# Performance work log

Measured on AMD Instinct MI355X. Metric: run time of the kernel, lower is better.

## Reference

```python
import jax, jax.numpy as jnp
from jax import lax
import numpy as np

D_MODEL = 1024
D_STATE = 16
D_CONV = 4
EXPAND = 2
D_INNER = EXPAND * D_MODEL          # 2048
DT_RANK = (D_MODEL + 15) // 16      # 64
B_SZ, SEQ = 2, 2048


def setup_inputs() -> dict:
    key = jax.random.key(0)
    ks = jax.random.split(key, 10)
    s = 0.02
    x = jax.random.normal(ks[0], (B_SZ, SEQ, D_MODEL), jnp.float32)
    ln_w = jnp.ones((D_MODEL,), jnp.float32)
    ln_b = jnp.zeros((D_MODEL,), jnp.float32)
    in_proj_w = jax.random.normal(ks[1], (2 * D_INNER, D_MODEL), jnp.float32) * s
    conv_w = jax.random.normal(ks[2], (D_INNER, 1, D_CONV), jnp.float32) * s
    conv_b = jnp.zeros((D_INNER,), jnp.float32)
    x_proj_w = jax.random.normal(ks[3], (DT_RANK + 2 * D_STATE, D_INNER), jnp.float32) * s
    dt_proj_w = jax.random.normal(ks[4], (D_INNER, DT_RANK), jnp.float32) * s
    dt_proj_b = jax.random.normal(ks[5], (D_INNER,), jnp.float32) * s
    # standard Mamba S4D-real init: A = -[1..d_state] per channel
    A_log = jnp.log(jnp.tile(jnp.arange(1, D_STATE + 1, dtype=jnp.float32), (D_INNER, 1)))
    D_param = jnp.ones((D_INNER,), jnp.float32)
    out_proj_w = jax.random.normal(ks[6], (D_MODEL, D_INNER), jnp.float32) * s
    return dict(x=x, ln_w=ln_w, ln_b=ln_b, in_proj_w=in_proj_w, conv_w=conv_w,
                conv_b=conv_b, x_proj_w=x_proj_w, dt_proj_w=dt_proj_w,
                dt_proj_b=dt_proj_b, A_log=A_log, D_param=D_param,
                out_proj_w=out_proj_w)


def _mamba_layer(x, ln_w, ln_b, in_proj_w, conv_w, conv_b, x_proj_w,
                 dt_proj_w, dt_proj_b, A_log, D_param, out_proj_w):
    # LayerNorm (eps=1e-5)
    mu = x.mean(-1, keepdims=True)
    var = ((x - mu) ** 2).mean(-1, keepdims=True)
    xn = (x - mu) * lax.rsqrt(var + 1e-5) * ln_w + ln_b

    # input projection -> gate + conv branch
    xz = jnp.einsum('bld,ed->ble', xn, in_proj_w)  # [B,L,2*D_INNER]
    x_in, z = jnp.split(xz, 2, axis=-1)

    # causal depthwise conv1d + SiLU
    xc = lax.conv_general_dilated(x_in.transpose(0, 2, 1), conv_w, (1,),
                                  [(D_CONV - 1, 0)],
                                  dimension_numbers=('NCH', 'OIH', 'NCH'),
                                  feature_group_count=D_INNER)
    xc = jax.nn.silu(xc + conv_b[None, :, None]).transpose(0, 2, 1)  # [B,L,D_INNER]

    # SSM parameters
    dbl = jnp.einsum('bld,ed->ble', xc, x_proj_w)  # [B,L,DT_RANK+2N]
    dt, Bm, Cm = jnp.split(dbl, [DT_RANK, DT_RANK + D_STATE], axis=-1)
    delta = jax.nn.softplus(jnp.einsum('blr,dr->bld', dt, dt_proj_w) + dt_proj_b)
    A = -jnp.exp(A_log)  # [D_INNER, D_STATE]

    # selective scan over time
    def step(h, inp):
        d_t, B_t, C_t, u_t = inp  # [B,D_INNER],[B,N],[B,N],[B,D_INNER]
        dA = jnp.exp(d_t[..., None] * A)                         # [B,D_INNER,N]
        h = dA * h + (d_t * u_t)[..., None] * B_t[:, None, :]    # [B,D_INNER,N]
        y = jnp.einsum('bdn,bn->bd', h, C_t)
        return h, y

    h0 = jnp.zeros((x.shape[0], D_INNER, D_STATE), x.dtype)
    _, ys = lax.scan(step, h0, (delta.transpose(1, 0, 2), Bm.transpose(1, 0, 2),
                                Cm.transpose(1, 0, 2), xc.transpose(1, 0, 2)))
    y = ys.transpose(1, 0, 2) + xc * D_param   # [B,L,D_INNER]

    y = y * jax.nn.silu(z)
    out = jnp.einsum('ble,de->bld', y, out_proj_w)
    # dropout p=0 (eval) -> identity; residual
    return x + out


def reference(x, ln_w, ln_b, in_proj_w, conv_w, conv_b, x_proj_w,
              dt_proj_w, dt_proj_b, A_log, D_param, out_proj_w):
    return _mamba_layer(x, ln_w, ln_b, in_proj_w, conv_w, conv_b, x_proj_w,
                        dt_proj_w, dt_proj_b, A_log, D_param, out_proj_w)
```

## Files before the change

### kernel.cpp

```cpp
#include <hip/hip_runtime.h>
#include <hip/hip_bf16.h>
#include <math.h>

#define D_MODEL 1024
#define D_INNER 2048
#define DT_RANK 64
#define D_STATE 16
#define BSZ 2
#define SEQ 2048
#define NROW (BSZ * SEQ)
#define NC 128
#define CL (SEQ / NC)
#define NCH (BSZ * D_INNER)
#define KSPLIT 16
#define KCH (D_INNER / KSPLIT)

typedef short bf16x8 __attribute__((ext_vector_type(8)));
typedef float f32x4 __attribute__((ext_vector_type(4)));

__device__ inline ushort f2bf(float f) {
    uint32_t u = __float_as_uint(f);
    return (ushort)((u + 0x7FFFu + ((u >> 16) & 1u)) >> 16);
}
__device__ inline float bf2f(ushort u) {
    return __uint_as_float(((uint32_t)u) << 16);
}

__device__ inline void gld_lds16(const void* g, void* l) {
    __builtin_amdgcn_global_load_lds(
        (__attribute__((address_space(1))) void*)g,
        (__attribute__((address_space(3))) void*)l, 16, 0, 0);
}

__global__ __launch_bounds__(256) void cvt_bf16(const float* __restrict__ in,
                                                ushort* __restrict__ out) {
    int i = blockIdx.x * 256 + threadIdx.x;
    float4 v = ((const float4*)in)[i];
    ushort4 o;
    o.x = f2bf(v.x); o.y = f2bf(v.y); o.z = f2bf(v.z); o.w = f2bf(v.w);
    ((ushort4*)out)[i] = o;
}

__global__ __launch_bounds__(256) void ln_kernel(const float* __restrict__ x,
                                                 const float* __restrict__ w,
                                                 const float* __restrict__ b,
                                                 ushort* __restrict__ xn) {
    int row = blockIdx.x;
    int tid = threadIdx.x;
    const float4* xr = (const float4*)(x + (size_t)row * D_MODEL);
    float4 v = xr[tid];
    float s  = v.x + v.y + v.z + v.w;
    float ss = v.x * v.x + v.y * v.y + v.z * v.z + v.w * v.w;
#pragma unroll
    for (int o = 32; o > 0; o >>= 1) {
        s  += __shfl_down(s, o);
        ss += __shfl_down(ss, o);
    }
    __shared__ float red[8];
    int wid = tid >> 6, lane = tid & 63;
    if (lane == 0) { red[wid] = s; red[4 + wid] = ss; }
    __syncthreads();
    s  = red[0] + red[1] + red[2] + red[3];
    ss = red[4] + red[5] + red[6] + red[7];
    float mu  = s * (1.0f / D_MODEL);
    float var = ss * (1.0f / D_MODEL) - mu * mu;
    float inv = rsqrtf(var + 1e-5f);
    float4 wv = ((const float4*)w)[tid];
    float4 bv = ((const float4*)b)[tid];
    ushort4 o4;
    o4.x = f2bf((v.x - mu) * inv * wv.x + bv.x);
    o4.y = f2bf((v.y - mu) * inv * wv.y + bv.y);
    o4.z = f2bf((v.z - mu) * inv * wv.z + bv.z);
    o4.w = f2bf((v.w - mu) * inv * wv.w + bv.w);
    ((ushort4*)(xn + (size_t)row * D_MODEL))[tid] = o4;
}

template <int MODE>
__global__ __launch_bounds__(256) void gemm_mfma(
    const ushort* __restrict__ A, int lda,
    const ushort* __restrict__ B, int ldb,
    float* __restrict__ C, ushort* __restrict__ Z0, ushort* __restrict__ Z1,
    int ldc, int splitN, const float* __restrict__ extra, int K) {
    __shared__ ushort lds[2][2][128 * 32];
    int tid = threadIdx.x;
    int w = tid >> 6, lane = tid & 63;
    int bm = blockIdx.y * 128, bn = blockIdx.x * 128;
    int wr = w >> 1, wc = w & 1;

    int srow = tid >> 2, sseg = (tid & 3) << 3;
    const ushort* Abase = A + (size_t)(bm + srow) * lda + sseg;
    const ushort* Bbase = B + (size_t)(bn + srow) * ldb + sseg;
    int l0 = w * 512;

    int frow = lane & 15, fk = (lane >> 4) << 3;
    f32x4 acc[4][4] = {};

#define STAGE(buf, k0)                                                        \
    do {                                                                      \
        gld_lds16(Abase + (k0),                     &lds[buf][0][l0]);        \
        gld_lds16(Abase + (size_t)64 * lda + (k0),  &lds[buf][0][2048 + l0]); \
        gld_lds16(Bbase + (k0),                     &lds[buf][1][l0]);        \
        gld_lds16(Bbase + (size_t)64 * ldb + (k0),  &lds[buf][1][2048 + l0]); \
    } while (0)

    int nk = K >> 5;
    int cur = 0;
    STAGE(0, 0);
    __syncthreads();
    for (int kt = 0; kt < nk; ++kt) {
        if (kt + 1 < nk) STAGE(cur ^ 1, (kt + 1) << 5);
        bf16x8 a[4], b[4];
#pragma unroll
        for (int m = 0; m < 4; ++m)
            a[m] = *(const bf16x8*)&lds[cur][0][(wr * 64 + m * 16 + frow) * 32 + fk];
#pragma unroll
        for (int n = 0; n < 4; ++n)
            b[n] = *(const bf16x8*)&lds[cur][1][(wc * 64 + n * 16 + frow) * 32 + fk];
#pragma unroll
        for (int m = 0; m < 4; ++m)
#pragma unroll
            for (int n = 0; n < 4; ++n)
                acc[m][n] = __builtin_amdgcn_mfma_f32_16x16x32_bf16(a[m], b[n], acc[m][n], 0, 0, 0);
        __syncthreads();
        cur ^= 1;
    }
#undef STAGE

    int rbase = bm + wr * 64 + ((lane >> 4) << 2);
    int cbase = bn + wc * 64 + (lane & 15);
#pragma unroll
    for (int m = 0; m < 4; ++m) {
#pragma unroll
        for (int n = 0; n < 4; ++n) {
            int gc = cbase + n * 16;
#pragma unroll
            for (int j = 0; j < 4; ++j) {
                int gr = rbase + m * 16 + j;
                float v = acc[m][n][j];
                if (MODE == 0) {
                    if (gc < splitN) Z0[(size_t)gr * ldc + gc] = f2bf(v);
                    else             Z1[(size_t)gr * ldc + (gc - splitN)] = f2bf(v);
                } else if (MODE == 1) {
                    v += extra[gc];
                    v = (v > 20.f) ? v : log1pf(__expf(v));
                    Z0[(size_t)gr * ldc + gc] = f2bf(v);
                } else {
                    C[(size_t)gr * ldc + gc] = v + extra[(size_t)gr * ldc + gc];
                }
            }
        }
    }
}

#define BM 64
#define BN 64
#define BK 16
__global__ __launch_bounds__(256) void gemm_b_split(const ushort* __restrict__ A,
                                                    const float* __restrict__ B,
                                                    float* __restrict__ part) {
    __shared__ float As[BK][BM];
    __shared__ float Bs[BK][BN];
    int bm = blockIdx.y * BM, bn = blockIdx.x * BN;
    int kc = blockIdx.z;
    int tid = threadIdx.x;
    int tx = tid & 15, ty = tid >> 4;
    int lrow = tid >> 2, lseg = (tid & 3) << 2;
    float acc[4][4] = {};

    int kbeg = kc * KCH;
    for (int k0 = kbeg; k0 < kbeg + KCH; k0 += BK) {
        ushort4 au = *(const ushort4*)(A + (size_t)(bm + lrow) * D_INNER + k0 + lseg);
        float4 av = make_float4(bf2f(au.x), bf2f(au.y), bf2f(au.z), bf2f(au.w));
        float4 bv = make_float4(0.f, 0.f, 0.f, 0.f);
        int bgr = bn + lrow;
        if (bgr < 96) bv = *(const float4*)(B + (size_t)bgr * D_INNER + k0 + lseg);
        __syncthreads();
        As[lseg + 0][lrow] = av.x; As[lseg + 1][lrow] = av.y;
        As[lseg + 2][lrow] = av.z; As[lseg + 3][lrow] = av.w;
        Bs[lseg + 0][lrow] = bv.x; Bs[lseg + 1][lrow] = bv.y;
        Bs[lseg + 2][lrow] = bv.z; Bs[lseg + 3][lrow] = bv.w;
        __syncthreads();
#pragma unroll
        for (int k = 0; k < BK; ++k) {
            float4 a4 = *(const float4*)&As[k][ty << 2];
            float4 b4 = *(const float4*)&Bs[k][tx << 2];
            float ar[4] = {a4.x, a4.y, a4.z, a4.w};
            float br[4] = {b4.x, b4.y, b4.z, b4.w};
#pragma unroll
            for (int i = 0; i < 4; ++i)
#pragma unroll
                for (int j = 0; j < 4; ++j) acc[i][j] += ar[i] * br[j];
        }
    }

    float* po = part + (size_t)kc * (NROW * 96);
#pragma unroll
    for (int i = 0; i < 4; ++i) {
        int gr = bm + (ty << 2) + i;
#pragma unroll
        for (int j = 0; j < 4; ++j) {
            int gc = bn + (tx << 2) + j;
            if (gc < 96) po[(size_t)gr * 96 + gc] = acc[i][j];
        }
    }
}

__global__ __launch_bounds__(256) void gemm_b_reduce(const float* __restrict__ part,
                                                     ushort* __restrict__ dbl) {
    int i = blockIdx.x * 256 + threadIdx.x;
    float s = 0.f;
#pragma unroll
    for (int kc = 0; kc < KSPLIT; ++kc)
        s += part[(size_t)kc * (NROW * 96) + i];
    dbl[i] = f2bf(s);
}

__global__ __launch_bounds__(256) void conv_silu(const ushort* __restrict__ xin,
                                                 const float* __restrict__ w,
                                                 const float* __restrict__ cb,
                                                 ushort* __restrict__ xc) {
    int idx = blockIdx.x * 256 + threadIdx.x;
    int d4 = idx & 511;
    int m  = idx >> 9;
    int l  = m & (SEQ - 1);
    int d  = d4 << 2;
    float4 w0 = ((const float4*)w)[d + 0];
    float4 w1 = ((const float4*)w)[d + 1];
    float4 w2 = ((const float4*)w)[d + 2];
    float4 w3 = ((const float4*)w)[d + 3];
    float wr0[4] = {w0.x, w0.y, w0.z, w0.w};
    float wr1[4] = {w1.x, w1.y, w1.z, w1.w};
    float wr2[4] = {w2.x, w2.y, w2.z, w2.w};
    float wr3[4] = {w3.x, w3.y, w3.z, w3.w};
    float ax = cb[d], ay = cb[d + 1], az = cb[d + 2], aw = cb[d + 3];
#pragma unroll
    for (int j = 0; j < 4; ++j) {
        if (l - 3 + j >= 0) {
            ushort4 xu = *(const ushort4*)(xin + (size_t)(m - 3 + j) * D_INNER + d);
            ax += wr0[j] * bf2f(xu.x);
            ay += wr1[j] * bf2f(xu.y);
            az += wr2[j] * bf2f(xu.z);
            aw += wr3[j] * bf2f(xu.w);
        }
    }
    ushort4 o;
    o.x = f2bf(ax / (1.f + __expf(-ax)));
    o.y = f2bf(ay / (1.f + __expf(-ay)));
    o.z = f2bf(az / (1.f + __expf(-az)));
    o.w = f2bf(aw / (1.f + __expf(-aw)));
    *(ushort4*)(xc + (size_t)m * D_INNER + d) = o;
}

#define EXP4(e, cj) \
    e.x = __expf(dt * cj.x); e.y = __expf(dt * cj.y); \
    e.z = __expf(dt * cj.z); e.w = __expf(dt * cj.w);
#define HUPD(hj, cj, Bv) { float4 e; EXP4(e, cj) \
    hj.x = e.x * hj.x + du * Bv.x; hj.y = e.y * hj.y + du * Bv.y; \
    hj.z = e.z * hj.z + du * Bv.z; hj.w = e.w * hj.w + du * Bv.w; }

__global__ __launch_bounds__(256) void scan_phase1(const ushort* __restrict__ delta,
                                                   const ushort* __restrict__ xc,
                                                   const ushort* __restrict__ dbl,
                                                   const float* __restrict__ A_log,
                                                   float* __restrict__ S,
                                                   float* __restrict__ sumdt) {
    __shared__ float bs[CL][16];
    int tid = threadIdx.x;
    int g = blockIdx.x * 256 + tid;
    int c = g & (NCH - 1);
    int k = g >> 12;
    int d = c & (D_INNER - 1);
    int b = c >> 11;
    size_t r0 = (size_t)b * SEQ + (size_t)k * CL;

    if (tid < CL * 4) {
        int t = tid >> 2, j = (tid & 3) << 2;
        ushort4 u4 = *(const ushort4*)(dbl + (r0 + t) * 96 + DT_RANK + j);
        bs[t][j + 0] = bf2f(u4.x); bs[t][j + 1] = bf2f(u4.y);
        bs[t][j + 2] = bf2f(u4.z); bs[t][j + 3] = bf2f(u4.w);
    }

    const float4* al = (const float4*)(A_log + d * D_STATE);
    float4 c0 = al[0], c1 = al[1], c2 = al[2], c3 = al[3];
    c0.x = -__expf(c0.x); c0.y = -__expf(c0.y); c0.z = -__expf(c0.z); c0.w = -__expf(c0.w);
    c1.x = -__expf(c1.x); c1.y = -__expf(c1.y); c1.z = -__expf(c1.z); c1.w = -__expf(c1.w);
    c2.x = -__expf(c2.x); c2.y = -__expf(c2.y); c2.z = -__expf(c2.z); c2.w = -__expf(c2.w);
    c3.x = -__expf(c3.x); c3.y = -__expf(c3.y); c3.z = -__expf(c3.z); c3.w = -__expf(c3.w);
    __syncthreads();

    const ushort* pd = delta + r0 * D_INNER + d;
    const ushort* pu = xc    + r0 * D_INNER + d;
    float4 h0 = {}, h1 = {}, h2 = {}, h3 = {};
    float sdt = 0.f;
#pragma unroll 4
    for (int t = 0; t < CL; ++t) {
        float dt = bf2f(*pd), u = bf2f(*pu);
        float4 B0 = *(const float4*)&bs[t][0];
        float4 B1 = *(const float4*)&bs[t][4];
        float4 B2 = *(const float4*)&bs[t][8];
        float4 B3 = *(const float4*)&bs[t][12];
        float du = dt * u;
        sdt += dt;
        HUPD(h0, c0, B0) HUPD(h1, c1, B1) HUPD(h2, c2, B2) HUPD(h3, c3, B3)
        pd += D_INNER; pu += D_INNER;
    }
    float4* So = (float4*)(S + ((size_t)g << 4));
    So[0] = h0; So[1] = h1; So[2] = h2; So[3] = h3;
    sumdt[g] = sdt;
}

__global__ __launch_bounds__(256) void scan_phase2(float* __restrict__ S,
                                                   const float* __restrict__ sumdt,
                                                   const float* __restrict__ A_log) {
    int g = blockIdx.x * 256 + threadIdx.x;
    int n = g & 15;
    int c = g >> 4;
    int d = c & (D_INNER - 1);
    float cn = -__expf(A_log[d * D_STATE + n]);
    float h = 0.f;
#pragma unroll 8
    for (int k = 0; k < NC; ++k) {
        int kc = (k << 12) | c;
        float P = __expf(sumdt[kc] * cn);
        size_t o = ((size_t)kc << 4) + n;
        float s = S[o];
        S[o] = h;
        h = P * h + s;
    }
}

__global__ __launch_bounds__(256) void scan_phase3(const ushort* __restrict__ delta,
                                                   const ushort* __restrict__ xc,
                                                   const ushort* __restrict__ dbl,
                                                   const ushort* __restrict__ zb,
                                                   const float* __restrict__ A_log,
                                                   const float* __restrict__ Dp,
                                                   const float* __restrict__ hin,
                                                   ushort* __restrict__ y) {
    __shared__ float bcs[CL][32];
    int tid = threadIdx.x;
    int g = blockIdx.x * 256 + tid;
    int c = g & (NCH - 1);
    int k = g >> 12;
    int d = c & (D_INNER - 1);
    int b = c >> 11;
    size_t r0 = (size_t)b * SEQ + (size_t)k * CL;

    if (tid < CL * 8) {
        int t = tid >> 3, j = (tid & 7) << 2;
        ushort4 u4 = *(const ushort4*)(dbl + (r0 + t) * 96 + DT_RANK + j);
        bcs[t][j + 0] = bf2f(u4.x); bcs[t][j + 1] = bf2f(u4.y);
        bcs[t][j + 2] = bf2f(u4.z); bcs[t][j + 3] = bf2f(u4.w);
    }

    const float4* al = (const float4*)(A_log + d * D_STATE);
    float4 c0 = al[0], c1 = al[1], c2 = al[2], c3 = al[3];
    c0.x = -__expf(c0.x); c0.y = -__expf(c0.y); c0.z = -__expf(c0.z); c0.w = -__expf(c0.w);
    c1.x = -__expf(c1.x); c1.y = -__expf(c1.y); c1.z = -__expf(c1.z); c1.w = -__expf(c1.w);
    c2.x = -__expf(c2.x); c2.y = -__expf(c2.y); c2.z = -__expf(c2.z); c2.w = -__expf(c2.w);
    c3.x = -__expf(c3.x); c3.y = -__expf(c3.y); c3.z = -__expf(c3.z); c3.w = -__expf(c3.w);
    float Dv = Dp[d];
    const float4* hi = (const float4*)(hin + ((size_t)g << 4));
    float4 h0 = hi[0], h1 = hi[1], h2 = hi[2], h3 = hi[3];
    __syncthreads();

    const ushort* pd = delta + r0 * D_INNER + d;
    const ushort* pu = xc    + r0 * D_INNER + d;
    const ushort* pz = zb    + r0 * D_INNER + d;
    ushort* py = y           + r0 * D_INNER + d;
#pragma unroll 4
    for (int t = 0; t < CL; ++t) {
        float dt = bf2f(*pd), u = bf2f(*pu);
        float4 B0 = *(const float4*)&bcs[t][0];
        float4 B1 = *(const float4*)&bcs[t][4];
        float4 B2 = *(const float4*)&bcs[t][8];
        float4 B3 = *(const float4*)&bcs[t][12];
        float4 C0 = *(const float4*)&bcs[t][16];
        float4 C1 = *(const float4*)&bcs[t][20];
        float4 C2 = *(const float4*)&bcs[t][24];
        float4 C3 = *(const float4*)&bcs[t][28];
        float du = dt * u;
        HUPD(h0, c0, B0) HUPD(h1, c1, B1) HUPD(h2, c2, B2) HUPD(h3, c3, B3)
        float acc = h0.x * C0.x + h0.y * C0.y + h0.z * C0.z + h0.w * C0.w
                  + h1.x * C1.x + h1.y * C1.y + h1.z * C1.z + h1.w * C1.w
                  + h2.x * C2.x + h2.y * C2.y + h2.z * C2.z + h2.w * C2.w
                  + h3.x * C3.x + h3.y * C3.y + h3.z * C3.z + h3.w * C3.w;
        float zv = bf2f(*pz);
        float sz = zv / (1.f + __expf(-zv));
        *py = f2bf((acc + u * Dv) * sz);
        pd += D_INNER; pu += D_INNER; pz += D_INNER; py += D_INNER;
    }
}

extern "C" void kernel_launch(void* const* d_in, const int* in_sizes, int n_in,
                              void* d_out, int out_size, void* d_ws, size_t ws_size,
                              hipStream_t stream) {
    const float* x       = (const float*)d_in[0];
    const float* ln_w    = (const float*)d_in[1];
    const float* ln_b    = (const float*)d_in[2];
    const float* in_proj = (const float*)d_in[3];
    const float* conv_w  = (const float*)d_in[4];
    const float* conv_b  = (const float*)d_in[5];
    const float* x_proj  = (const float*)d_in[6];
    const float* dt_w    = (const float*)d_in[7];
    const float* dt_b    = (const float*)d_in[8];
    const float* A_log   = (const float*)d_in[9];
    const float* Dp      = (const float*)d_in[10];
    const float* out_w   = (const float*)d_in[11];
    float* out = (float*)d_out;

    char* ws = (char*)d_ws;
    const size_t MB = 1024ull * 1024ull;
    ushort* xn_bf    = (ushort*)(ws);
    ushort* w_in_bf  = (ushort*)(ws + 8 * MB);
    float*  Shin     = (float*)(ws);
    ushort* x_in_bf  = (ushort*)(ws + 16 * MB);
    ushort* zbuf_bf  = (ushort*)(ws + 32 * MB);
    ushort* xc_bf    = (ushort*)(ws + 48 * MB);
    ushort* dbl_bf   = (ushort*)(ws + 64 * MB);
    ushort* dt_w_bf  = (ushort*)(ws + 65 * MB);
    ushort* delta_bf = (ushort*)(ws + 66 * MB);
    ushort* y_bf     = (ushort*)(ws + 82 * MB);
    float*  sumdt    = (float*)(ws + 98 * MB);
    float*  part     = (float*)(ws + 100 * MB);
    ushort* w_out_bf = (ushort*)(ws + 124 * MB);

    cvt_bf16<<<(2 * D_INNER * D_MODEL / 4) / 256, 256, 0, stream>>>(in_proj, w_in_bf);
    cvt_bf16<<<(D_MODEL * D_INNER / 4) / 256, 256, 0, stream>>>(out_w, w_out_bf);
    cvt_bf16<<<(D_INNER * DT_RANK / 4) / 256, 256, 0, stream>>>(dt_w, dt_w_bf);

    ln_kernel<<<NROW, 256, 0, stream>>>(x, ln_w, ln_b, xn_bf);

    gemm_mfma<0><<<dim3(4096 / 128, NROW / 128), 256, 0, stream>>>(
        xn_bf, D_MODEL, w_in_bf, D_MODEL, nullptr, x_in_bf, zbuf_bf,
        D_INNER, D_INNER, nullptr, D_MODEL);

    conv_silu<<<(NROW * (D_INNER / 4)) / 256, 256, 0, stream>>>(x_in_bf, conv_w, conv_b, xc_bf);

    gemm_b_split<<<dim3(2, NROW / BM, KSPLIT), 256, 0, stream>>>(xc_bf, x_proj, part);
    gemm_b_reduce<<<(NROW * 96) / 256, 256, 0, stream>>>(part, dbl_bf);

    gemm_mfma<1><<<dim3(D_INNER / 128, NROW / 128), 256, 0, stream>>>(
        dbl_bf, 96, dt_w_bf, DT_RANK, nullptr, delta_bf, nullptr,
        D_INNER, 0, dt_b, DT_RANK);

    scan_phase1<<<(NCH * NC) / 256, 256, 0, stream>>>(
        delta_bf, xc_bf, dbl_bf, A_log, Shin, sumdt);
    scan_phase2<<<(NCH * D_STATE) / 256, 256, 0, stream>>>(Shin, sumdt, A_log);
    scan_phase3<<<(NCH * NC) / 256, 256, 0, stream>>>(
        delta_bf, xc_bf, dbl_bf, zbuf_bf, A_log, Dp, Shin, y_bf);

    gemm_mfma<2><<<dim3(D_MODEL / 128, NROW / 128), 256, 0, stream>>>(
        y_bf, D_INNER, w_out_bf, D_INNER, out, nullptr, nullptr,
        D_MODEL, 0, x, D_INNER);
}
```

Measured before the change: 396.2 us.

## Split-K the output projection, swizzle GEMM blocks, merge weight conversions

The output projection GEMM becomes split-K across four slices, writing fp32 partials that a new reduce kernel sums together with the residual input. This raises the workgroup count from one per CU to four per CU. All MFMA GEMMs also remap block ids in groups of eight (an XCD-style swizzle) to change cache locality, and the three weight-conversion launches are merged into one kernel. The cost is about 64MB of extra partial-sum writes and reads, plus one extra launch for the reduce.

Result: no change. 389.5 us (-1.7%).

```diff
diff --git a/kernel.cpp b/kernel.cpp
--- a/kernel.cpp
+++ b/kernel.cpp
@@ -14,6 +14,7 @@
 #define NCH (BSZ * D_INNER)
 #define KSPLIT 16
 #define KCH (D_INNER / KSPLIT)
+#define DSPLIT 4
 
 typedef short bf16x8 __attribute__((ext_vector_type(8)));
 typedef float f32x4 __attribute__((ext_vector_type(4)));
@@ -32,13 +33,24 @@
         (__attribute__((address_space(3))) void*)l, 16, 0, 0);
 }
 
-__global__ __launch_bounds__(256) void cvt_bf16(const float* __restrict__ in,
-                                                ushort* __restrict__ out) {
+#define CVT_N1 (2 * D_INNER * D_MODEL / 4)
+#define CVT_N2 (D_MODEL * D_INNER / 4)
+#define CVT_N3 (D_INNER * DT_RANK / 4)
+__global__ __launch_bounds__(256) void cvt_all(const float* __restrict__ a,
+                                               const float* __restrict__ b,
+                                               const float* __restrict__ c,
+                                               ushort* __restrict__ oa,
+                                               ushort* __restrict__ ob,
+                                               ushort* __restrict__ oc) {
     int i = blockIdx.x * 256 + threadIdx.x;
-    float4 v = ((const float4*)in)[i];
+    const float* src; ushort* dst; int j;
+    if (i < CVT_N1)               { src = a; dst = oa; j = i; }
+    else if (i < CVT_N1 + CVT_N2) { src = b; dst = ob; j = i - CVT_N1; }
+    else                          { src = c; dst = oc; j = i - CVT_N1 - CVT_N2; }
+    float4 v = ((const float4*)src)[j];
     ushort4 o;
     o.x = f2bf(v.x); o.y = f2bf(v.y); o.z = f2bf(v.z); o.w = f2bf(v.w);
-    ((ushort4*)out)[i] = o;
+    ((ushort4*)dst)[j] = o;
 }
 
 __global__ __launch_bounds__(256) void ln_kernel(const float* __restrict__ x,
@@ -80,16 +92,23 @@
     const ushort* __restrict__ A, int lda,
     const ushort* __restrict__ B, int ldb,
     float* __restrict__ C, ushort* __restrict__ Z0, ushort* __restrict__ Z1,
-    int ldc, int splitN, const float* __restrict__ extra, int K) {
+    int ldc, int splitN, const float* __restrict__ extra, int K, size_t zstride) {
     __shared__ ushort lds[2][2][128 * 32];
     int tid = threadIdx.x;
     int w = tid >> 6, lane = tid & 63;
-    int bm = blockIdx.y * 128, bn = blockIdx.x * 128;
+
+    int nwg = gridDim.x * gridDim.y;
+    int bid = blockIdx.y * gridDim.x + blockIdx.x;
+    int cpx = nwg >> 3;
+    int swz = (bid & 7) * cpx + (bid >> 3);
+    int bx = swz % gridDim.x, by = swz / gridDim.x;
+    int bm = by * 128, bn = bx * 128;
     int wr = w >> 1, wc = w & 1;
 
+    int kofs = (MODE == 3) ? blockIdx.z * K : 0;
     int srow = tid >> 2, sseg = (tid & 3) << 3;
-    const ushort* Abase = A + (size_t)(bm + srow) * lda + sseg;
-    const ushort* Bbase = B + (size_t)(bn + srow) * ldb + sseg;
+    const ushort* Abase = A + (size_t)(bm + srow) * lda + sseg + kofs;
+    const ushort* Bbase = B + (size_t)(bn + srow) * ldb + sseg + kofs;
     int l0 = w * 512;
 
     int frow = lane & 15, fk = (lane >> 4) << 3;
@@ -126,6 +145,7 @@
     }
 #undef STAGE
 
+    float* Cz = (MODE == 3) ? (C + (size_t)blockIdx.z * zstride) : C;
     int rbase = bm + wr * 64 + ((lane >> 4) << 2);
     int cbase = bn + wc * 64 + (lane & 15);
 #pragma unroll
@@ -144,12 +164,27 @@
                     v += extra[gc];
                     v = (v > 20.f) ? v : log1pf(__expf(v));
                     Z0[(size_t)gr * ldc + gc] = f2bf(v);
+                } else if (MODE == 2) {
+                    C[(size_t)gr * ldc + gc] = v + extra[(size_t)gr * ldc + gc];
                 } else {
-                    C[(size_t)gr * ldc + gc] = v + extra[(size_t)gr * ldc + gc];
+                    Cz[(size_t)gr * ldc + gc] = v;
                 }
             }
         }
     }
+}
+
+__global__ __launch_bounds__(256) void gemm_d_reduce(const float* __restrict__ part,
+                                                     const float* __restrict__ x,
+                                                     float* __restrict__ out) {
+    int i = blockIdx.x * 256 + threadIdx.x;
+    float4 s = ((const float4*)x)[i];
+#pragma unroll
+    for (int z = 0; z < DSPLIT; ++z) {
+        float4 p = ((const float4*)(part + (size_t)z * (NROW * D_MODEL)))[i];
+        s.x += p.x; s.y += p.y; s.z += p.z; s.w += p.w;
+    }
+    ((float4*)out)[i] = s;
 }
 
 #define BM 64
@@ -414,6 +449,7 @@
     ushort* xn_bf    = (ushort*)(ws);
     ushort* w_in_bf  = (ushort*)(ws + 8 * MB);
     float*  Shin     = (float*)(ws);
+    float*  part_d   = (float*)(ws);
     ushort* x_in_bf  = (ushort*)(ws + 16 * MB);
     ushort* zbuf_bf  = (ushort*)(ws + 32 * MB);
     ushort* xc_bf    = (ushort*)(ws + 48 * MB);
@@ -422,27 +458,26 @@
     ushort* delta_bf = (ushort*)(ws + 66 * MB);
     ushort* y_bf     = (ushort*)(ws + 82 * MB);
     float*  sumdt    = (float*)(ws + 98 * MB);
-    float*  part     = (float*)(ws + 100 * MB);
+    float*  part_b   = (float*)(ws + 100 * MB);
     ushort* w_out_bf = (ushort*)(ws + 124 * MB);
 
-    cvt_bf16<<<(2 * D_INNER * D_MODEL / 4) / 256, 256, 0, stream>>>(in_proj, w_in_bf);
-    cvt_bf16<<<(D_MODEL * D_INNER / 4) / 256, 256, 0, stream>>>(out_w, w_out_bf);
-    cvt_bf16<<<(D_INNER * DT_RANK / 4) / 256, 256, 0, stream>>>(dt_w, dt_w_bf);
+    cvt_all<<<(CVT_N1 + CVT_N2 + CVT_N3) / 256, 256, 0, stream>>>(
+        in_proj, out_w, dt_w, w_in_bf, w_out_bf, dt_w_bf);
 
     ln_kernel<<<NROW, 256, 0, stream>>>(x, ln_w, ln_b, xn_bf);
 
     gemm_mfma<0><<<dim3(4096 / 128, NROW / 128), 256, 0, stream>>>(
         xn_bf, D_MODEL, w_in_bf, D_MODEL, nullptr, x_in_bf, zbuf_bf,
-        D_INNER, D_INNER, nullptr, D_MODEL);
+        D_INNER, D_INNER, nullptr, D_MODEL, 0);
 
     conv_silu<<<(NROW * (D_INNER / 4)) / 256, 256, 0, stream>>>(x_in_bf, conv_w, conv_b, xc_bf);
 
-    gemm_b_split<<<dim3(2, NROW / BM, KSPLIT), 256, 0, stream>>>(xc_bf, x_proj, part);
-    gemm_b_reduce<<<(NROW * 96) / 256, 256, 0, stream>>>(part, dbl_bf);
+    gemm_b_split<<<dim3(2, NROW / BM, KSPLIT), 256, 0, stream>>>(xc_bf, x_proj, part_b);
+    gemm_b_reduce<<<(NROW * 96) / 256, 256, 0, stream>>>(part_b, dbl_bf);
 
     gemm_mfma<1><<<dim3(D_INNER / 128, NROW / 128), 256, 0, stream>>>(
         dbl_bf, 96, dt_w_bf, DT_RANK, nullptr, delta_bf, nullptr,
-        D_INNER, 0, dt_b, DT_RANK);
+        D_INNER, 0, dt_b, DT_RANK, 0);
 
     scan_phase1<<<(NCH * NC) / 256, 256, 0, stream>>>(
         delta_bf, xc_bf, dbl_bf, A_log, Shin, sumdt);
@@ -450,7 +485,8 @@
     scan_phase3<<<(NCH * NC) / 256, 256, 0, stream>>>(
         delta_bf, xc_bf, dbl_bf, zbuf_bf, A_log, Dp, Shin, y_bf);
 
-    gemm_mfma<2><<<dim3(D_MODEL / 128, NROW / 128), 256, 0, stream>>>(
-        y_bf, D_INNER, w_out_bf, D_INNER, out, nullptr, nullptr,
-        D_MODEL, 0, x, D_INNER);
-}
+    gemm_mfma<3><<<dim3(D_MODEL / 128, NROW / 128, DSPLIT), 256, 0, stream>>>(
+        y_bf, D_INNER, w_out_bf, D_INNER, part_d, nullptr, nullptr,
+        D_MODEL, 0, nullptr, D_INNER / DSPLIT, (size_t)NROW * D_MODEL);
+    gemm_d_reduce<<<(NROW * D_MODEL / 4) / 256, 256, 0, stream>>>(part_d, x, out);
+}
```
